# Kernel optimization log

Measured on AMD Instinct MI355X. Metric: run time of the kernel, lower is better.

Reference implementation:

```python
import jax, jax.numpy as jnp
import numpy as np

L, S, D, H, DL, V, B = 8, 1024, 768, 12, 64, 512, 8
NB, NM = 32, 64  # big_bird neighbours, global memory columns


def _bigbird_mask():
    i = np.arange(S)[:, None]
    j = np.arange(S)[None, :]
    m = ((np.abs(i - j) <= NB) | (j < NM)) & (j <= i)  # window + global cols, then tril
    return jnp.asarray(m)[None, None]  # [1,1,S,S]


def _ln(x, g, b):
    mu = x.mean(-1, keepdims=True)
    var = ((x - mu) ** 2).mean(-1, keepdims=True)
    return (x - mu) / jnp.sqrt(var + 1e-5) * g + b


def setup_inputs() -> dict:
    key = jax.random.key(0)
    ks = jax.random.split(key, 16)
    s = 0.02
    d = {
        'x': jax.random.randint(ks[0], (B, S), 0, V),
        'targets': jax.random.randint(ks[1], (B, S), 0, V),
        'wte': jax.random.normal(ks[2], (V, D), jnp.float32) * s,
        'pos': jnp.zeros((1, S, D), jnp.float32),
        'ln1_g': jnp.ones((L, D)), 'ln1_b': jnp.zeros((L, D)),
        'wq': jax.random.normal(ks[3], (L, D, D)) * s, 'bq': jnp.zeros((L, D)),
        'wk': jax.random.normal(ks[4], (L, D, D)) * s, 'bk': jnp.zeros((L, D)),
        'wv': jax.random.normal(ks[5], (L, D, D)) * s, 'bv': jnp.zeros((L, D)),
        'ln2_g': jnp.ones((L, D)), 'ln2_b': jnp.zeros((L, D)),
        'w1': jax.random.normal(ks[6], (L, D, 4 * D)) * s, 'b1': jnp.zeros((L, 4 * D)),
        'w2': jax.random.normal(ks[7], (L, 4 * D, D)) * s, 'b2': jnp.zeros((L, D)),
        'lnf_g': jnp.ones((D,)), 'lnf_b': jnp.zeros((D,)),
        'w_out': jax.random.normal(ks[8], (D, V)) * s,
    }
    return d


def _forward(x, targets, wte, pos, ln1_g, ln1_b, wq, bq, wk, bk, wv, bv,
             ln2_g, ln2_b, w1, b1, w2, b2, lnf_g, lnf_b, w_out):
    mask = _bigbird_mask()
    h = wte[x] + pos  # [B,S,D]
    scale = DL ** -0.5
    neg_inf = jnp.array(float('-inf'), h.dtype)
    for l in range(L):
        a = _ln(h, ln1_g[l], ln1_b[l])
        q = (a @ wq[l] + bq[l]).reshape(B, S, H, DL).transpose(0, 2, 1, 3)
        k = (a @ wk[l] + bk[l]).reshape(B, S, H, DL).transpose(0, 2, 1, 3)
        v = (a @ wv[l] + bv[l]).reshape(B, S, H, DL).transpose(0, 2, 1, 3)
        att = jnp.einsum('bhqd,bhkd->bhqk', q, k) * scale
        att = jnp.where(mask, att, neg_inf)
        att = jax.nn.softmax(att, axis=-1)
        z = jnp.einsum('bhqk,bhkd->bhqd', att, v)
        z = z.transpose(0, 2, 1, 3).reshape(B, S, D)
        h = h + z  # note: W_0 is defined in the torch module but never applied
        m = _ln(h, ln2_g[l], ln2_b[l])
        h = h + jax.nn.gelu(m @ w1[l] + b1[l], approximate=False) @ w2[l] + b2[l]
    h = _ln(h, lnf_g, lnf_b)
    pred = h @ w_out  # [B,S,V]
    logp = jax.nn.log_softmax(pred.reshape(B * S, V), axis=-1)
    loss = -jnp.take_along_axis(logp, targets.reshape(-1, 1), axis=1).mean()
    return pred, loss


def reference(x, targets, wte, pos, ln1_g, ln1_b, wq, bq, wk, bk, wv, bv,
              ln2_g, ln2_b, w1, b1, w2, b2, lnf_g, lnf_b, w_out):
    return _forward(x, targets, wte, pos, ln1_g, ln1_b, wq, bq, wk, bk, wv, bv,
                    ln2_g, ln2_b, w1, b1, w2, b2, lnf_g, lnf_b, w_out)
```

## Files before the change

kernel.cpp:

```cpp
#include <hip/hip_runtime.h>
#include <hip/hip_bf16.h>

#define DEV __device__ __forceinline__

typedef __attribute__((ext_vector_type(8))) short short8;
typedef __attribute__((ext_vector_type(4))) float f32x4;

DEV unsigned short f2bf(float f){
  unsigned int u = __builtin_bit_cast(unsigned int, f);
  u += 0x7FFFu + ((u >> 16) & 1u);
  return (unsigned short)(u >> 16);
}

DEV void gld_lds16(const void* g, void* l){
  __builtin_amdgcn_global_load_lds((const __attribute__((address_space(1))) void*)g,
                                   (__attribute__((address_space(3))) void*)l, 16, 0, 0);
}

__global__ void k_embed(const int* __restrict__ x, const float* __restrict__ wte,
                        const float* __restrict__ pos, float* __restrict__ h){
  int i4 = (blockIdx.x * 256 + threadIdx.x) * 4;
  int row = i4 / 768, d = i4 - row * 768;
  int s = row & 1023;
  f32x4 a = *(const f32x4*)(wte + (size_t)x[row] * 768 + d);
  f32x4 p = *(const f32x4*)(pos + s * 768 + d);
  #pragma unroll
  for(int e = 0; e < 4; e++) a[e] += p[e];
  *(f32x4*)(h + i4) = a;
}

__global__ void k_ln(const float* __restrict__ src, const float* __restrict__ g,
                     const float* __restrict__ b, unsigned short* __restrict__ out){
  int w = threadIdx.x >> 6, lane = threadIdx.x & 63;
  int row = blockIdx.x * 4 + w;
  const float* p = src + (size_t)row * 768;
  f32x4 v[3];
  #pragma unroll
  for(int k = 0; k < 3; k++) v[k] = *(const f32x4*)(p + k * 256 + lane * 4);
  float s = 0.f, sq = 0.f;
  #pragma unroll
  for(int k = 0; k < 3; k++)
    #pragma unroll
    for(int e = 0; e < 4; e++){ s += v[k][e]; sq += v[k][e] * v[k][e]; }
  #pragma unroll
  for(int m = 32; m >= 1; m >>= 1){ s += __shfl_xor(s, m); sq += __shfl_xor(sq, m); }
  float mu  = s * (1.0f / 768.0f);
  float inv = rsqrtf(sq * (1.0f / 768.0f) - mu * mu + 1e-5f);
  unsigned short* o = out + (size_t)row * 768;
  #pragma unroll
  for(int k = 0; k < 3; k++){
    f32x4 gg = *(const f32x4*)(g + k * 256 + lane * 4);
    f32x4 bb = *(const f32x4*)(b + k * 256 + lane * 4);
    unsigned long long pk =
        (unsigned long long)f2bf((v[k][0] - mu) * inv * gg[0] + bb[0]) |
        ((unsigned long long)f2bf((v[k][1] - mu) * inv * gg[1] + bb[1]) << 16) |
        ((unsigned long long)f2bf((v[k][2] - mu) * inv * gg[2] + bb[2]) << 32) |
        ((unsigned long long)f2bf((v[k][3] - mu) * inv * gg[3] + bb[3]) << 48);
    *(unsigned long long*)(o + k * 256 + lane * 4) = pk;
  }
}

DEV void tr_tile256(float (*tl)[33], const float* __restrict__ src, unsigned short* __restrict__ dst,
                    int R, int C, int tx, int ty, int tid){
  int r0 = ty * 256, c0 = tx * 32;
  const float* sp = src + (size_t)(r0 + tid) * C + c0;
  #pragma unroll
  for(int e = 0; e < 32; e++) tl[tid][e] = sp[e];
  __syncthreads();
  int lx = tid & 31, ly = tid >> 5;
  #pragma unroll
  for(int j = 0; j < 4; j++){
    int oc = ly + 8 * j;
    short8 pk;
    #pragma unroll
    for(int e = 0; e < 8; e++) pk[e] = (short)f2bf(tl[8 * lx + e][oc]);
    *(short8*)(dst + (size_t)(c0 + oc) * R + r0 + 8 * lx) = pk;
  }
}

__global__ void k_convert_all(const float* __restrict__ wq, const float* __restrict__ wk,
                              const float* __restrict__ wv, const float* __restrict__ w1,
                              const float* __restrict__ w2, const float* __restrict__ bq,
                              const float* __restrict__ bk, const float* __restrict__ bv,
                              unsigned short* __restrict__ wall, float* __restrict__ qkvb,
                              int l0, int slot0){
  __shared__ float tl[256][33];
  int l = l0 + blockIdx.y, slot = slot0 + blockIdx.y;
  int bid = blockIdx.x, tid = threadIdx.x;
  unsigned short* wqkv_t = wall + (size_t)slot * 6488064;
  unsigned short* w1_t   = wqkv_t + 1769472;
  unsigned short* w2_t   = w1_t + 2359296;
  float* qb = qkvb + slot * 2304;
  const float* wq_l = wq + (size_t)l * 589824;
  const float* wk_l = wk + (size_t)l * 589824;
  const float* wv_l = wv + (size_t)l * 589824;
  const float* w1_l = w1 + (size_t)l * 2359296;
  const float* w2_l = w2 + (size_t)l * 2359296;
  if(bid < 216){
    int which = bid / 72, t = bid - which * 72;
    const float* src = which == 0 ? wq_l : which == 1 ? wk_l : wv_l;
    tr_tile256(tl, src, wqkv_t + (size_t)which * 589824, 768, 768, t % 24, t / 24, tid);
  } else if(bid < 216 + 288){
    int t = bid - 216;
    tr_tile256(tl, w1_l, w1_t, 768, 3072, t % 96, t / 96, tid);
  } else if(bid < 216 + 576){
    int t = bid - 504;
    tr_tile256(tl, w2_l, w2_t, 3072, 768, t % 24, t / 24, tid);
  } else {
    for(int i = tid; i < 768; i += 256){
      qb[i] = bq[l * 768 + i]; qb[768 + i] = bk[l * 768 + i]; qb[1536 + i] = bv[l * 768 + i];
    }
  }
}

__global__ void k_transpose(const float* __restrict__ src, unsigned short* __restrict__ dst,
                            int R, int C){
  __shared__ float tl[256][33];
  int nx = C / 32;
  tr_tile256(tl, src, dst, R, C, blockIdx.x % nx, blockIdx.x / nx, threadIdx.x);
}

template<int EPI, int MW, int NB>
__global__ __launch_bounds__(MW * 128, 4)
void k_gemm(const unsigned short* __restrict__ A, const unsigned short* __restrict__ Bt,
            const float* __restrict__ bias, int K,
            float* __restrict__ fout, unsigned short* __restrict__ o0,
            unsigned short* __restrict__ o1, unsigned short* __restrict__ o2){
  constexpr int THREADS = MW * 128;
  constexpr int AL = 4;
  constexpr int BL = (2 * NB) / MW;
  __shared__ unsigned short As[MW * 64 * 64];
  __shared__ unsigned short Bs[NB * 32 * 64];
  int tid = threadIdx.x, w = tid >> 6, lane = tid & 63;
  int l15 = lane & 15, l4 = lane >> 4;
  int nbx = gridDim.x;
  int bid = blockIdx.y * nbx + blockIdx.x;
  int cpx = (nbx * gridDim.y) >> 3;
  int sid = (bid & 7) * cpx + (bid >> 3);
  int bm = sid / nbx, bn = sid - bm * nbx;
  int N = nbx * NB * 32;
  int wr = w >> 1, wc = w & 1;
  f32x4 acc[4][NB] = {};
  int rowA[AL], colA[AL], rowB[BL], colB[BL];
  #pragma unroll
  for(int i = 0; i < AL; i++){
    int o = i * THREADS * 16 + tid * 16;
    int r = o >> 7, ch = (o >> 4) & 7;
    rowA[i] = r; colA[i] = ((ch ^ (r & 7)) << 3);
  }
  #pragma unroll
  for(int i = 0; i < BL; i++){
    int o = i * THREADS * 16 + tid * 16;
    int r = o >> 7, ch = (o >> 4) & 7;
    rowB[i] = r; colB[i] = ((ch ^ (r & 7)) << 3);
  }
  const size_t aBase = (size_t)bm * (MW * 64);
  const size_t bBase = (size_t)bn * (NB * 32);
  for(int kt = 0; kt < K; kt += 64){
    #pragma unroll
    for(int i = 0; i < AL; i++)
      gld_lds16(A + (aBase + rowA[i]) * K + kt + colA[i],
                (char*)As + i * THREADS * 16 + tid * 16);
    #pragma unroll
    for(int i = 0; i < BL; i++)
      gld_lds16(Bt + (bBase + rowB[i]) * K + kt + colB[i],
                (char*)Bs + i * THREADS * 16 + tid * 16);
    __syncthreads();
    #pragma unroll
    for(int s = 0; s < 2; s++){
      short8 af[4], bfr[NB];
      #pragma unroll
      for(int m = 0; m < 4; m++){
        int r = wr * 64 + m * 16 + l15;
        int ch = s * 4 + l4;
        af[m] = *(const short8*)(As + r * 64 + ((ch ^ (r & 7)) << 3));
      }
      #pragma unroll
      for(int n = 0; n < NB; n++){
        int r = wc * (NB * 16) + n * 16 + l15;
        int ch = s * 4 + l4;
        bfr[n] = *(const short8*)(Bs + r * 64 + ((ch ^ (r & 7)) << 3));
      }
      #pragma unroll
      for(int m = 0; m < 4; m++)
        #pragma unroll
        for(int n = 0; n < NB; n++)
          acc[m][n] = __builtin_amdgcn_mfma_f32_16x16x32_bf16(af[m], bfr[n], acc[m][n], 0, 0, 0);
    }
    __syncthreads();
  }
  int r0 = bm * (MW * 64) + wr * 64 + (l4 << 2);
  int c0 = bn * (NB * 32) + wc * (NB * 16) + l15;
  if(EPI == 0){
    unsigned short* dstn[NB];
    float bvn[NB];
    #pragma unroll
    for(int n = 0; n < NB; n++){
      int col = c0 + n * 16;
      bvn[n] = bias[col];
      int which = col / 768, cc = col - which * 768;
      int hd = cc >> 6, dl = cc & 63;
      unsigned short* dst = which == 0 ? o0 : which == 1 ? o1 : o2;
      dstn[n] = dst + (size_t)hd * 65536 + dl;
    }
    #pragma unroll
    for(int m = 0; m < 4; m++){
      #pragma unroll
      for(int j = 0; j < 4; j++){
        int row = r0 + m * 16 + j;
        int bb = row >> 10, sp = row & 1023;
        size_t ro = ((size_t)bb * 12288 + sp) * 64;
        #pragma unroll
        for(int n = 0; n < NB; n++)
          dstn[n][ro] = f2bf(acc[m][n][j] + bvn[n]);
      }
    }
  } else {
    float bvn[NB];
    #pragma unroll
    for(int n = 0; n < NB; n++) bvn[n] = (EPI == 3) ? 0.0f : bias[c0 + n * 16];
    #pragma unroll
    for(int m = 0; m < 4; m++){
      #pragma unroll
      for(int j = 0; j < 4; j++){
        int row = r0 + m * 16 + j;
        #pragma unroll
        for(int n = 0; n < NB; n++){
          int col = c0 + n * 16;
          float v = acc[m][n][j] + bvn[n];
          if(EPI == 1){
            float t = v * (1.5957691f + 0.07135481f * v * v);
            float gl = v * __builtin_amdgcn_rcpf(1.0f + __expf(-t));
            o0[(size_t)row * N + col] = f2bf(gl);
          } else if(EPI == 2){
            fout[(size_t)row * 768 + col] += v;
          } else {
            fout[(size_t)row * 512 + col] = v;
          }
        }
      }
    }
  }
}

__global__ __launch_bounds__(256)
void k_attn(const unsigned short* __restrict__ qg, const unsigned short* __restrict__ kg,
            const unsigned short* __restrict__ vg, float* __restrict__ h){
  __shared__ unsigned short Vt[64 * 256];
  __shared__ unsigned short Ps[4][32 * 128];
  int qb = blockIdx.x, bh = blockIdx.y;
  int tid = threadIdx.x, w = tid >> 6, lane = tid & 63;
  int b = bh / 12, hd = bh - b * 12;
  int wbase = qb * 128 - 32;
  const unsigned short* vb = vg + (size_t)bh * 1024 * 64;
  for(int u = tid; u < 224 * 8; u += 256){
    int slot = u >> 3, c8 = u & 7;
    int j = slot < 64 ? slot : wbase + (slot - 64);
    if(j < 0) j = 0;
    short8 vv = *(const short8*)(vb + (size_t)j * 64 + c8 * 8);
    #pragma unroll
    for(int e = 0; e < 8; e++){
      int d = c8 * 8 + e;
      Vt[d * 256 + (((slot >> 3) ^ (d & 7)) << 3) + (slot & 7)] = (unsigned short)vv[e];
    }
  }
  __syncthreads();
  int i0 = qb * 128 + 32 * w;
  const unsigned short* qrow = qg + (size_t)bh * 1024 * 64;
  const unsigned short* krow = kg + (size_t)bh * 1024 * 64;
  short8 qf[2][2];
  #pragma unroll
  for(int m = 0; m < 2; m++)
    #pragma unroll
    for(int s = 0; s < 2; s++)
      qf[m][s] = *(const short8*)(qrow + (size_t)(i0 + m * 16 + (lane & 15)) * 64 + s * 32 + ((lane >> 4) << 3));
  f32x4 sacc[2][8] = {};
  #pragma unroll
  for(int n = 0; n < 8; n++){
    int jk = (n < 4) ? (n * 16 + (lane & 15))
                     : (wbase + 32 * w + (n - 4) * 16 + (lane & 15));
    int jc = jk < 0 ? 0 : jk;
    const unsigned short* kr = krow + (size_t)jc * 64 + ((lane >> 4) << 3);
    short8 k0 = *(const short8*)(kr);
    short8 k1 = *(const short8*)(kr + 32);
    #pragma unroll
    for(int m = 0; m < 2; m++){
      sacc[m][n] = __builtin_amdgcn_mfma_f32_16x16x32_bf16(qf[m][0], k0, sacc[m][n], 0, 0, 0);
      sacc[m][n] = __builtin_amdgcn_mfma_f32_16x16x32_bf16(qf[m][1], k1, sacc[m][n], 0, 0, 0);
    }
  }
  #pragma unroll
  for(int m = 0; m < 2; m++)
    #pragma unroll
    for(int n = 0; n < 8; n++){
      int s_ = n * 16 + (lane & 15);
      int jkey = (n < 4) ? s_ : (wbase + 32 * w + (s_ - 64));
      #pragma unroll
      for(int j = 0; j < 4; j++){
        int qi = i0 + m * 16 + ((lane >> 4) << 2) + j;
        bool ok = (n < 4) ? (jkey <= qi)
                          : (jkey >= 64 && jkey <= qi && (qi - jkey) <= 32);
        sacc[m][n][j] = ok ? sacc[m][n][j] * 0.125f : -1e30f;
      }
    }
  float rsum[2][4];
  #pragma unroll
  for(int m = 0; m < 2; m++)
    #pragma unroll
    for(int j = 0; j < 4; j++){
      float mx = sacc[m][0][j];
      #pragma unroll
      for(int n = 1; n < 8; n++) mx = fmaxf(mx, sacc[m][n][j]);
      mx = fmaxf(mx, __shfl_xor(mx, 1)); mx = fmaxf(mx, __shfl_xor(mx, 2));
      mx = fmaxf(mx, __shfl_xor(mx, 4)); mx = fmaxf(mx, __shfl_xor(mx, 8));
      float sm = 0.f;
      #pragma unroll
      for(int n = 0; n < 8; n++){
        float e = expf(sacc[m][n][j] - mx);
        sacc[m][n][j] = e;
        sm += e;
      }
      sm += __shfl_xor(sm, 1); sm += __shfl_xor(sm, 2);
      sm += __shfl_xor(sm, 4); sm += __shfl_xor(sm, 8);
      rsum[m][j] = sm;
    }
  unsigned short* Pw = Ps[w];
  #pragma unroll
  for(int m = 0; m < 2; m++)
    #pragma unroll
    for(int n = 0; n < 8; n++){
      int s_ = n * 16 + (lane & 15);
      #pragma unroll
      for(int j = 0; j < 4; j++){
        int ql = m * 16 + ((lane >> 4) << 2) + j;
        Pw[ql * 128 + (((s_ >> 3) ^ (ql & 7)) << 3) + (s_ & 7)] = f2bf(sacc[m][n][j]);
      }
    }
  f32x4 oacc[2][4] = {};
  #pragma unroll
  for(int s = 0; s < 4; s++){
    short8 pa[2];
    #pragma unroll
    for(int m = 0; m < 2; m++){
      int ql = m * 16 + (lane & 15);
      int ch = s * 4 + (lane >> 4);
      pa[m] = *(const short8*)(Pw + ql * 128 + ((ch ^ (ql & 7)) << 3));
    }
    int kk = s * 32 + ((lane >> 4) << 3);
    int slot0 = kk < 64 ? kk : 64 + 32 * w + (kk - 64);
    #pragma unroll
    for(int n = 0; n < 4; n++){
      int d = n * 16 + (lane & 15);
      short8 vv = *(const short8*)(Vt + d * 256 + (((slot0 >> 3) ^ (d & 7)) << 3));
      #pragma unroll
      for(int m = 0; m < 2; m++)
        oacc[m][n] = __builtin_amdgcn_mfma_f32_16x16x32_bf16(pa[m], vv, oacc[m][n], 0, 0, 0);
    }
  }
  #pragma unroll
  for(int m = 0; m < 2; m++)
    #pragma unroll
    for(int j = 0; j < 4; j++){
      int ql = m * 16 + ((lane >> 4) << 2) + j;
      float inv = 1.0f / rsum[m][j];
      size_t base = ((size_t)(b * 1024 + i0 + ql)) * 768 + hd * 64;
      #pragma unroll
      for(int n = 0; n < 4; n++){
        int d = n * 16 + (lane & 15);
        h[base + d] += oacc[m][n][j] * inv;
      }
    }
}

__global__ void k_rowloss(const float* __restrict__ pred, const int* __restrict__ tgt,
                          float* __restrict__ rowloss){
  int row = blockIdx.x * 4 + (threadIdx.x >> 6);
  int lane = threadIdx.x & 63;
  const float* p = pred + (size_t)row * 512 + lane * 8;
  float v[8];
  #pragma unroll
  for(int i = 0; i < 8; i++) v[i] = p[i];
  float mx = v[0];
  #pragma unroll
  for(int i = 1; i < 8; i++) mx = fmaxf(mx, v[i]);
  #pragma unroll
  for(int m = 1; m < 64; m <<= 1) mx = fmaxf(mx, __shfl_xor(mx, m));
  float se = 0.f;
  #pragma unroll
  for(int i = 0; i < 8; i++) se += expf(v[i] - mx);
  #pragma unroll
  for(int m = 1; m < 64; m <<= 1) se += __shfl_xor(se, m);
  int t = tgt[row];
  float pt = 0.f;
  int base = lane * 8;
  #pragma unroll
  for(int i = 0; i < 8; i++) pt = (t == base + i) ? v[i] : pt;
  #pragma unroll
  for(int m = 1; m < 64; m <<= 1) pt += __shfl_xor(pt, m);
  if(lane == 0) rowloss[row] = -(pt - mx - logf(se));
}

__global__ void k_lossfinal(const float* __restrict__ rowloss, float* __restrict__ out){
  int tid = threadIdx.x;
  float s = 0.f;
  for(int i = tid; i < 8192; i += 256) s += rowloss[i];
  #pragma unroll
  for(int m = 32; m >= 1; m >>= 1) s += __shfl_xor(s, m);
  __shared__ float red[4];
  if((tid & 63) == 0) red[tid >> 6] = s;
  __syncthreads();
  if(tid == 0) out[0] = (red[0] + red[1] + red[2] + red[3]) * (1.0f / 8192.0f);
}

extern "C" void kernel_launch(void* const* d_in, const int* in_sizes, int n_in,
                              void* d_out, int out_size, void* d_ws, size_t ws_size,
                              hipStream_t stream){
  const int*   x       = (const int*)d_in[0];
  const int*   targets = (const int*)d_in[1];
  const float* wte     = (const float*)d_in[2];
  const float* pos     = (const float*)d_in[3];
  const float* ln1_g   = (const float*)d_in[4];
  const float* ln1_b   = (const float*)d_in[5];
  const float* wq      = (const float*)d_in[6];
  const float* bq      = (const float*)d_in[7];
  const float* wk      = (const float*)d_in[8];
  const float* bk      = (const float*)d_in[9];
  const float* wv      = (const float*)d_in[10];
  const float* bv      = (const float*)d_in[11];
  const float* ln2_g   = (const float*)d_in[12];
  const float* ln2_b   = (const float*)d_in[13];
  const float* w1      = (const float*)d_in[14];
  const float* b1      = (const float*)d_in[15];
  const float* w2      = (const float*)d_in[16];
  const float* b2      = (const float*)d_in[17];
  const float* lnf_g   = (const float*)d_in[18];
  const float* lnf_b   = (const float*)d_in[19];
  const float* w_out   = (const float*)d_in[20];
  float* out = (float*)d_out;

  char* ws = (char*)d_ws;
  float*          h      = (float*)ws;
  unsigned short* a_bf   = (unsigned short*)(ws + 25165824);
  char*           big    = ws + 37748736;
  unsigned short* qbf    = (unsigned short*)big;
  unsigned short* kbf    = (unsigned short*)(big + 12582912);
  unsigned short* vbf    = (unsigned short*)(big + 25165824);
  unsigned short* tbf    = (unsigned short*)big;
  bool mega = ws_size >= 192782336ull;
  unsigned short* wall   = (unsigned short*)(ws + 88080384);
  size_t wend = 88080384ull + (mega ? 103809024ull : 12976128ull);
  unsigned short* wout_t = (unsigned short*)(ws + wend);
  float*          qkvb   = (float*)(ws + wend + 786432);
  float*          rowls  = (float*)(ws + wend + 786432 + (mega ? 73728 : 9216));

  if(mega){
    k_convert_all<<<dim3(793, 4), 256, 0, stream>>>(wq, wk, wv, w1, w2, bq, bk, bv,
                                                    wall, qkvb, 0, 0);
    k_convert_all<<<dim3(793, 4), 256, 0, stream>>>(wq, wk, wv, w1, w2, bq, bk, bv,
                                                    wall, qkvb, 4, 4);
  }
  k_transpose<<<48, 256, 0, stream>>>(w_out, wout_t, 768, 512);
  k_embed<<<6144, 256, 0, stream>>>(x, wte, pos, h);
  for(int l = 0; l < 8; l++){
    if(!mega)
      k_convert_all<<<dim3(793, 1), 256, 0, stream>>>(wq, wk, wv, w1, w2, bq, bk, bv,
                                                      wall, qkvb, l, 0);
    int slot = mega ? l : 0;
    unsigned short* wqkv_l = wall + (size_t)slot * 6488064;
    unsigned short* w1_l   = wqkv_l + 1769472;
    unsigned short* w2_l   = w1_l + 2359296;
    float*          qkvb_l = qkvb + slot * 2304;
    k_ln<<<2048, 256, 0, stream>>>(h, ln1_g + l * 768, ln1_b + l * 768, a_bf);
    k_gemm<0,4,4><<<dim3(18, 32), 512, 0, stream>>>(a_bf, wqkv_l, qkvb_l, 768, nullptr, qbf, kbf, vbf);
    k_attn<<<dim3(8, 96), 256, 0, stream>>>(qbf, kbf, vbf, h);
    k_ln<<<2048, 256, 0, stream>>>(h, ln2_g + l * 768, ln2_b + l * 768, a_bf);
    k_gemm<1,4,4><<<dim3(24, 32), 512, 0, stream>>>(a_bf, w1_l, b1 + l * 3072, 768, nullptr, tbf, nullptr, nullptr);
    k_gemm<2,2,2><<<dim3(12, 64), 256, 0, stream>>>(tbf, w2_l, b2 + l * 768, 3072, h, nullptr, nullptr, nullptr);
  }
  k_ln<<<2048, 256, 0, stream>>>(h, lnf_g, lnf_b, a_bf);
  k_gemm<3,2,2><<<dim3(8, 64), 256, 0, stream>>>(a_bf, wout_t, nullptr, 768, out, nullptr, nullptr, nullptr);
  k_rowloss<<<2048, 256, 0, stream>>>(out, targets, rowls);
  k_lossfinal<<<1, 256, 0, stream>>>(rowls, out + 4194304);
}
```

Before: 1.583 ms.

## Add 256x256-tile pipelined GEMM kernel for QKV and FFN1 projections

Adds a new GEMM kernel with 256x256 output tiles and 8 waves. It double-buffers A and B halves in LDS using direct global-to-LDS loads, interleaves staging with MFMA phases, and uses barriers and s_setprio to overlap memory with compute. The QKV and W1 GEMMs move to this kernel, and the old kernel keeps only the residual-add and logits epilogues. The larger tiles should cut LDS and global traffic per FLOP, at the cost of fewer blocks (288/384) on a 256-CU device and higher register pressure.

Measured after the change: 1.787 ms. 12.9% more time.

```diff
diff --git a/kernel.cpp b/kernel.cpp
--- a/kernel.cpp
+++ b/kernel.cpp
@@ -120,12 +120,137 @@
   tr_tile256(tl, src, dst, R, C, blockIdx.x % nx, blockIdx.x / nx, threadIdx.x);
 }
 
+#define STG_A(BUF,H,KT) { \
+    gld_lds16(A  + (aB + (H)*128 + sr0) * K + (KT) + so0, (char*)Ah[BUF][H] + tid*16); \
+    gld_lds16(A  + (aB + (H)*128 + sr1) * K + (KT) + so0, (char*)Ah[BUF][H] + 8192 + tid*16); }
+#define STG_B(BUF,H,KT) { \
+    gld_lds16(Bt + (bB + (H)*128 + sr0) * K + (KT) + so0, (char*)Bh[BUF][H] + tid*16); \
+    gld_lds16(Bt + (bB + (H)*128 + sr1) * K + (KT) + so0, (char*)Bh[BUF][H] + 8192 + tid*16); }
+#define RD_A(BUF, MOFF) \
+  _Pragma("unroll") for(int m=0;m<4;m++) _Pragma("unroll") for(int ks=0;ks<2;ks++){ \
+    int r = (MOFF) + m*16 + l15; \
+    af[m][ks] = *(const short8*)(Ah[BUF][wr] + r*64 + ((((ks<<2)+l4) ^ (r&7))<<3)); }
+#define RD_B(BUF, HALF, DST) \
+  _Pragma("unroll") for(int n=0;n<2;n++) _Pragma("unroll") for(int ks=0;ks<2;ks++){ \
+    int r = n*64 + (wc<<4) + l15; \
+    DST[n][ks] = *(const short8*)(Bh[BUF][HALF] + r*64 + ((((ks<<2)+l4) ^ (r&7))<<3)); }
+#define MM(MB, NBASE, BF) \
+  _Pragma("unroll") for(int ks=0;ks<2;ks++) \
+  _Pragma("unroll") for(int m=0;m<4;m++) \
+  _Pragma("unroll") for(int n=0;n<2;n++) \
+    acc[(MB)+m][(NBASE)+n] = __builtin_amdgcn_mfma_f32_16x16x32_bf16( \
+        af[m][ks], BF[n][ks], acc[(MB)+m][(NBASE)+n], 0, 0, 0);
+#define PH_PRE()  __builtin_amdgcn_s_barrier(); \
+                  asm volatile("s_waitcnt lgkmcnt(0)" ::: "memory"); \
+                  __builtin_amdgcn_s_setprio(1);
+#define PH_POST() __builtin_amdgcn_s_setprio(0); __builtin_amdgcn_s_barrier();
+
+template<int EPI>
+__global__ __launch_bounds__(512, 2)
+void k_g256(const unsigned short* __restrict__ A, const unsigned short* __restrict__ Bt,
+            const float* __restrict__ bias, int K, int T,
+            unsigned short* __restrict__ o0, unsigned short* __restrict__ o1,
+            unsigned short* __restrict__ o2){
+  __shared__ unsigned short Ah[2][2][8192];
+  __shared__ unsigned short Bh[2][2][8192];
+  int tid = threadIdx.x, lane = tid & 63, w = tid >> 6;
+  int l15 = lane & 15, l4 = lane >> 4;
+  int wr = w >> 2, wc = w & 3;
+  int nbx = gridDim.x;
+  int bid = blockIdx.y * nbx + blockIdx.x;
+  int cpx = (nbx * gridDim.y) >> 3;
+  int sid = (bid & 7) * cpx + (bid >> 3);
+  int bm = sid / nbx, bn = sid - bm * nbx;
+  int sr0 = tid >> 3, sc = tid & 7;
+  int sr1 = 64 + sr0;
+  int so0 = ((sc ^ (sr0 & 7)) << 3);
+  const size_t aB = (size_t)bm * 256, bB = (size_t)bn * 256;
+  f32x4 acc[8][4] = {};
+  short8 af[4][2], bfLo[2][2], bfHi[2][2];
+
+  STG_A(0,0,0) STG_A(0,1,0) STG_B(0,0,0) STG_B(0,1,0)
+  {
+    int k1 = (T > 1 ? 1 : 0) * 64;
+    STG_B(1,0,k1) STG_B(1,1,k1)
+  }
+  asm volatile("s_waitcnt vmcnt(4)" ::: "memory");
+  __builtin_amdgcn_s_barrier();
+
+  for(int t = 0; t < T; t++){
+    int b = t & 1;
+    int kt1 = ((t+1) < T ? (t+1) : (T-1)) * 64;
+    int kt2 = ((t+2) < T ? (t+2) : (T-1)) * 64;
+    RD_A(b, 0) RD_B(b, 0, bfLo)
+    STG_A(b^1, 0, kt1)
+    PH_PRE() MM(0,0,bfLo) PH_POST()
+    RD_B(b, 1, bfHi)
+    STG_A(b^1, 1, kt1)
+    PH_PRE() MM(0,2,bfHi) PH_POST()
+    RD_A(b, 64)
+    STG_B(b, 0, kt2)
+    PH_PRE() MM(4,0,bfLo) PH_POST()
+    STG_B(b, 1, kt2)
+    __builtin_amdgcn_s_barrier();
+    asm volatile("s_waitcnt lgkmcnt(0)" ::: "memory");
+    __builtin_amdgcn_s_setprio(1); MM(4,2,bfHi) __builtin_amdgcn_s_setprio(0);
+    asm volatile("s_waitcnt vmcnt(4)" ::: "memory");
+    __builtin_amdgcn_s_barrier();
+  }
+
+  int r0 = bm * 256 + wr * 128 + (l4 << 2);
+  int c0 = bn * 256 + (wc << 4) + l15;
+  if(EPI == 0){
+    unsigned short* dstn[4];
+    float bvn[4];
+    #pragma unroll
+    for(int n = 0; n < 4; n++){
+      int col = c0 + n * 64;
+      bvn[n] = bias[col];
+      int which = col / 768, cc = col - which * 768;
+      int hd = cc >> 6, dl = cc & 63;
+      unsigned short* dst = which == 0 ? o0 : which == 1 ? o1 : o2;
+      dstn[n] = dst + (size_t)hd * 65536 + dl;
+    }
+    #pragma unroll
+    for(int m = 0; m < 8; m++){
+      #pragma unroll
+      for(int j = 0; j < 4; j++){
+        int row = r0 + m * 16 + j;
+        int bb2 = row >> 10, sp = row & 1023;
+        size_t ro = ((size_t)bb2 * 12288 + sp) * 64;
+        #pragma unroll
+        for(int n = 0; n < 4; n++)
+          dstn[n][ro] = f2bf(acc[m][n][j] + bvn[n]);
+      }
+    }
+  } else {
+    int N = nbx * 256;
+    float bvn[4];
+    #pragma unroll
+    for(int n = 0; n < 4; n++) bvn[n] = bias[c0 + n * 64];
+    #pragma unroll
+    for(int m = 0; m < 8; m++){
+      #pragma unroll
+      for(int j = 0; j < 4; j++){
+        int row = r0 + m * 16 + j;
+        #pragma unroll
+        for(int n = 0; n < 4; n++){
+          int col = c0 + n * 64;
+          float v = acc[m][n][j] + bvn[n];
+          float tt = v * (1.5957691f + 0.07135481f * v * v);
+          float gl = v * __builtin_amdgcn_rcpf(1.0f + __expf(-tt));
+          o0[(size_t)row * N + col] = f2bf(gl);
+        }
+      }
+    }
+  }
+}
+
 template<int EPI, int MW, int NB>
 __global__ __launch_bounds__(MW * 128, 4)
 void k_gemm(const unsigned short* __restrict__ A, const unsigned short* __restrict__ Bt,
             const float* __restrict__ bias, int K,
-            float* __restrict__ fout, unsigned short* __restrict__ o0,
-            unsigned short* __restrict__ o1, unsigned short* __restrict__ o2){
+            float* __restrict__ fout, unsigned short* __restrict__ o0){
   constexpr int THREADS = MW * 128;
   constexpr int AL = 4;
   constexpr int BL = (2 * NB) / MW;
@@ -138,7 +263,6 @@
   int cpx = (nbx * gridDim.y) >> 3;
   int sid = (bid & 7) * cpx + (bid >> 3);
   int bm = sid / nbx, bn = sid - bm * nbx;
-  int N = nbx * NB * 32;
   int wr = w >> 1, wc = w & 1;
   f32x4 acc[4][NB] = {};
   int rowA[AL], colA[AL], rowB[BL], colB[BL];
@@ -191,52 +315,22 @@
   }
   int r0 = bm * (MW * 64) + wr * 64 + (l4 << 2);
   int c0 = bn * (NB * 32) + wc * (NB * 16) + l15;
-  if(EPI == 0){
-    unsigned short* dstn[NB];
-    float bvn[NB];
-    #pragma unroll
-    for(int n = 0; n < NB; n++){
-      int col = c0 + n * 16;
-      bvn[n] = bias[col];
-      int which = col / 768, cc = col - which * 768;
-      int hd = cc >> 6, dl = cc & 63;
-      unsigned short* dst = which == 0 ? o0 : which == 1 ? o1 : o2;
-      dstn[n] = dst + (size_t)hd * 65536 + dl;
-    }
-    #pragma unroll
-    for(int m = 0; m < 4; m++){
-      #pragma unroll
-      for(int j = 0; j < 4; j++){
-        int row = r0 + m * 16 + j;
-        int bb = row >> 10, sp = row & 1023;
-        size_t ro = ((size_t)bb * 12288 + sp) * 64;
-        #pragma unroll
-        for(int n = 0; n < NB; n++)
-          dstn[n][ro] = f2bf(acc[m][n][j] + bvn[n]);
-      }
-    }
-  } else {
-    float bvn[NB];
-    #pragma unroll
-    for(int n = 0; n < NB; n++) bvn[n] = (EPI == 3) ? 0.0f : bias[c0 + n * 16];
-    #pragma unroll
-    for(int m = 0; m < 4; m++){
-      #pragma unroll
-      for(int j = 0; j < 4; j++){
-        int row = r0 + m * 16 + j;
-        #pragma unroll
-        for(int n = 0; n < NB; n++){
-          int col = c0 + n * 16;
-          float v = acc[m][n][j] + bvn[n];
-          if(EPI == 1){
-            float t = v * (1.5957691f + 0.07135481f * v * v);
-            float gl = v * __builtin_amdgcn_rcpf(1.0f + __expf(-t));
-            o0[(size_t)row * N + col] = f2bf(gl);
-          } else if(EPI == 2){
-            fout[(size_t)row * 768 + col] += v;
-          } else {
-            fout[(size_t)row * 512 + col] = v;
-          }
+  float bvn[NB];
+  #pragma unroll
+  for(int n = 0; n < NB; n++) bvn[n] = (EPI == 3) ? 0.0f : bias[c0 + n * 16];
+  #pragma unroll
+  for(int m = 0; m < 4; m++){
+    #pragma unroll
+    for(int j = 0; j < 4; j++){
+      int row = r0 + m * 16 + j;
+      #pragma unroll
+      for(int n = 0; n < NB; n++){
+        int col = c0 + n * 16;
+        float v = acc[m][n][j] + bvn[n];
+        if(EPI == 2){
+          fout[(size_t)row * 768 + col] += v;
+        } else {
+          fout[(size_t)row * 512 + col] = v;
         }
       }
     }
@@ -471,14 +565,14 @@
     unsigned short* w2_l   = w1_l + 2359296;
     float*          qkvb_l = qkvb + slot * 2304;
     k_ln<<<2048, 256, 0, stream>>>(h, ln1_g + l * 768, ln1_b + l * 768, a_bf);
-    k_gemm<0,4,4><<<dim3(18, 32), 512, 0, stream>>>(a_bf, wqkv_l, qkvb_l, 768, nullptr, qbf, kbf, vbf);
+    k_g256<0><<<dim3(9, 32), 512, 0, stream>>>(a_bf, wqkv_l, qkvb_l, 768, 12, qbf, kbf, vbf);
     k_attn<<<dim3(8, 96), 256, 0, stream>>>(qbf, kbf, vbf, h);
     k_ln<<<2048, 256, 0, stream>>>(h, ln2_g + l * 768, ln2_b + l * 768, a_bf);
-    k_gemm<1,4,4><<<dim3(24, 32), 512, 0, stream>>>(a_bf, w1_l, b1 + l * 3072, 768, nullptr, tbf, nullptr, nullptr);
-    k_gemm<2,2,2><<<dim3(12, 64), 256, 0, stream>>>(tbf, w2_l, b2 + l * 768, 3072, h, nullptr, nullptr, nullptr);
+    k_g256<1><<<dim3(12, 32), 512, 0, stream>>>(a_bf, w1_l, b1 + l * 3072, 768, 12, tbf, nullptr, nullptr);
+    k_gemm<2,2,2><<<dim3(12, 64), 256, 0, stream>>>(tbf, w2_l, b2 + l * 768, 3072, h, nullptr);
   }
   k_ln<<<2048, 256, 0, stream>>>(h, lnf_g, lnf_b, a_bf);
-  k_gemm<3,2,2><<<dim3(8, 64), 256, 0, stream>>>(a_bf, wout_t, nullptr, 768, out, nullptr, nullptr, nullptr);
+  k_gemm<3,2,2><<<dim3(8, 64), 256, 0, stream>>>(a_bf, wout_t, nullptr, 768, out, nullptr);
   k_rowloss<<<2048, 256, 0, stream>>>(out, targets, rowls);
   k_lossfinal<<<1, 256, 0, stream>>>(rowls, out + 4194304);
 }
```
